# Performance work log

Hardware: AMD Instinct MI355X
Metric: run time of the kernel (lower is better)

The kernel has to match this reference:

```python
import jax, jax.numpy as jnp
import numpy as np

B = 32
N_IN = 65536
N_OUT = 65536
NNZ = 2097152  # ~32 connections per output unit


def setup_inputs() -> dict:
    key = jax.random.key(0)
    k_x, k_w, k_r, k_c = jax.random.split(key, 4)
    x = jax.random.normal(k_x, (B, N_IN), dtype=jnp.float32)
    # weight init mirrors torch: randn * (init_scale / sqrt(mean_fan_in))
    init_scale = 0.01
    fan_in_mean = float(NNZ) / float(N_OUT)
    weight = jax.random.normal(k_w, (NNZ,), dtype=jnp.float32) * (init_scale / np.sqrt(fan_in_mean))
    bias = jnp.zeros((N_OUT,), dtype=jnp.float32)
    # rows are sorted (concatenated per output j in the original __init__)
    rows = jnp.sort(jax.random.randint(k_r, (NNZ,), 0, N_OUT, dtype=jnp.int64))
    cols = jax.random.randint(k_c, (NNZ,), 0, N_IN, dtype=jnp.int64)
    return {"x": x, "weight": weight, "bias": bias, "rows": rows, "cols": cols, "N_out": N_OUT}


def reference(x, weight, bias, rows, cols, N_out):
    # gather input columns per connection, scale by per-edge weight: (B, nnz)
    weighted = x[:, cols] * weight[None, :]
    # batched scatter-add by output row: segment_sum over edges -> (N_out, B) -> (B, N_out)
    out = jax.ops.segment_sum(weighted.T, rows, num_segments=N_out,
                              indices_are_sorted=True).T
    return out + bias[None, :]
```

## Files before the change

### kernel.cpp

```cpp
#include <hip/hip_runtime.h>


typedef unsigned int u32;

static __device__ __forceinline__ u32 f2bf_bits(float f) {
  u32 b = __builtin_bit_cast(u32, f);
  return (b + 0x7fffu + ((b >> 16) & 1u)) >> 16;
}
static __device__ __forceinline__ float bf_lo(u32 u) {
  return __builtin_bit_cast(float, u << 16);
}
static __device__ __forceinline__ float bf_hi(u32 u) {
  return __builtin_bit_cast(float, u & 0xffff0000u);
}

__global__ __launch_bounds__(256) void prep_kernel(
    const float* __restrict__ x, u32* __restrict__ xTb,
    const int* __restrict__ rows, int* __restrict__ row_ptr,
    int n_in, int n_out, int nnz, int tblocks) {
  if ((int)blockIdx.x < tblocks) {
    __shared__ float t[32][65];
    int c0 = blockIdx.x * 64;
    if (c0 + 64 <= n_in) {
      const float4* x4 = (const float4*)x;
      for (int idx = threadIdx.x; idx < 32 * 16; idx += 256) {
        int b = idx >> 4, q = idx & 15;
        float4 v = x4[((size_t)b * n_in + c0) / 4 + q];
        t[b][q * 4 + 0] = v.x; t[b][q * 4 + 1] = v.y;
        t[b][q * 4 + 2] = v.z; t[b][q * 4 + 3] = v.w;
      }
    } else {
      for (int idx = threadIdx.x; idx < 32 * 64; idx += 256) {
        int b = idx >> 6, cl = idx & 63;
        int c = c0 + cl;
        t[b][cl] = (c < n_in) ? x[(size_t)b * n_in + c] : 0.f;
      }
    }
    __syncthreads();
    for (int idx = threadIdx.x; idx < 64 * 16; idx += 256) {
      int cl = idx >> 4, bp = idx & 15;
      int c = c0 + cl;
      if (c < n_in) {
        u32 v = f2bf_bits(t[2 * bp][cl]) | (f2bf_bits(t[2 * bp + 1][cl]) << 16);
        xTb[(size_t)c * 16 + bp] = v;
      }
    }
  } else {
    int j = ((int)blockIdx.x - tblocks) * 256 + threadIdx.x;
    if (j <= n_out) {
      int lo = 0, hi = nnz;
      while (lo < hi) { int m = (lo + hi) >> 1; if (rows[m] < j) lo = m + 1; else hi = m; }
      row_ptr[j] = lo;
    }
  }
}

__global__ __launch_bounds__(256) void ll_main_bf16_kernel(
    const uint4* __restrict__ xTb4,
    const float* __restrict__ wgt,
    const float4* __restrict__ bias4,
    const int* __restrict__ cols,
    const int* __restrict__ row_ptr,
    float4* __restrict__ out4, int n_out) {
  __shared__ float tile[32][65];
  int tid = threadIdx.x;
  int g = tid >> 2;
  int l = tid & 3;
  int jb = blockIdx.x * 64;
  int j = jb + g;
  float a0 = 0, a1 = 0, a2 = 0, a3 = 0, a4 = 0, a5 = 0, a6 = 0, a7 = 0;
  if (j < n_out) {
    int s = row_ptr[j], e = row_ptr[j + 1];
    int last = e - 1;
    for (int base = s; base < e; base += 8) {
      int i1 = min(base + 1, last), i2 = min(base + 2, last), i3 = min(base + 3, last);
      int i4 = min(base + 4, last), i5 = min(base + 5, last), i6 = min(base + 6, last);
      int i7 = min(base + 7, last);
      int c0 = cols[base], c1 = cols[i1], c2 = cols[i2], c3 = cols[i3];
      int c4 = cols[i4], c5 = cols[i5], c6 = cols[i6], c7 = cols[i7];
      float w0 = wgt[base];
      float w1 = (base + 1 <= last) ? wgt[i1] : 0.f;
      float w2 = (base + 2 <= last) ? wgt[i2] : 0.f;
      float w3 = (base + 3 <= last) ? wgt[i3] : 0.f;
      float w4 = (base + 4 <= last) ? wgt[i4] : 0.f;
      float w5 = (base + 5 <= last) ? wgt[i5] : 0.f;
      float w6 = (base + 6 <= last) ? wgt[i6] : 0.f;
      float w7 = (base + 7 <= last) ? wgt[i7] : 0.f;
      uint4 v0 = xTb4[(size_t)c0 * 4 + l];
      uint4 v1 = xTb4[(size_t)c1 * 4 + l];
      uint4 v2 = xTb4[(size_t)c2 * 4 + l];
      uint4 v3 = xTb4[(size_t)c3 * 4 + l];
      uint4 v4 = xTb4[(size_t)c4 * 4 + l];
      uint4 v5 = xTb4[(size_t)c5 * 4 + l];
      uint4 v6 = xTb4[(size_t)c6 * 4 + l];
      uint4 v7 = xTb4[(size_t)c7 * 4 + l];
#define EDGE(V, W) \
      a0 = fmaf(W, bf_lo(V.x), a0); a1 = fmaf(W, bf_hi(V.x), a1); \
      a2 = fmaf(W, bf_lo(V.y), a2); a3 = fmaf(W, bf_hi(V.y), a3); \
      a4 = fmaf(W, bf_lo(V.z), a4); a5 = fmaf(W, bf_hi(V.z), a5); \
      a6 = fmaf(W, bf_lo(V.w), a6); a7 = fmaf(W, bf_hi(V.w), a7);
      EDGE(v0, w0) EDGE(v1, w1) EDGE(v2, w2) EDGE(v3, w3)
      EDGE(v4, w4) EDGE(v5, w5) EDGE(v6, w6) EDGE(v7, w7)
#undef EDGE
    }
  }
  int b0 = l * 8;
  tile[b0 + 0][g] = a0; tile[b0 + 1][g] = a1; tile[b0 + 2][g] = a2; tile[b0 + 3][g] = a3;
  tile[b0 + 4][g] = a4; tile[b0 + 5][g] = a5; tile[b0 + 6][g] = a6; tile[b0 + 7][g] = a7;
  __syncthreads();
  for (int slot = tid; slot < 32 * 16; slot += 256) {
    int bb = slot >> 4, q = slot & 15;
    int jj = jb + q * 4;
    if (jj + 3 < n_out) {
      float4 bv = bias4[jj / 4];
      float4 o;
      o.x = tile[bb][q * 4 + 0] + bv.x;
      o.y = tile[bb][q * 4 + 1] + bv.y;
      o.z = tile[bb][q * 4 + 2] + bv.z;
      o.w = tile[bb][q * 4 + 3] + bv.w;
      out4[((size_t)bb * n_out + jj) / 4] = o;
    } else {
      float* out = (float*)out4;
      const float* bias = (const float*)bias4;
      for (int d = 0; d < 4; ++d)
        if (jj + d < n_out)
          out[(size_t)bb * n_out + jj + d] = tile[bb][q * 4 + d] + bias[jj + d];
    }
  }
}

__global__ __launch_bounds__(256) void transpose_x_kernel(
    const float* __restrict__ x, float* __restrict__ xT, int n_in) {
  __shared__ float t[32][65];
  int c0 = blockIdx.x * 64;
  for (int idx = threadIdx.x; idx < 32 * 64; idx += 256) {
    int b = idx >> 6, cl = idx & 63;
    int c = c0 + cl;
    t[b][cl] = (c < n_in) ? x[(size_t)b * n_in + c] : 0.0f;
  }
  __syncthreads();
  for (int idx = threadIdx.x; idx < 64 * 32; idx += 256) {
    int cl = idx >> 5, b = idx & 31;
    int c = c0 + cl;
    if (c < n_in) xT[(size_t)c * 32 + b] = t[b][cl];
  }
}

__global__ __launch_bounds__(256) void build_rowptr_bs_kernel(
    const int* __restrict__ rows, int* __restrict__ row_ptr, int nnz, int n_out) {
  int j = blockIdx.x * blockDim.x + threadIdx.x;
  if (j > n_out) return;
  int lo = 0, hi = nnz;
  while (lo < hi) { int m = (lo + hi) >> 1; if (rows[m] < j) lo = m + 1; else hi = m; }
  row_ptr[j] = lo;
}

__global__ __launch_bounds__(256) void ll_main4_kernel(
    const float4* __restrict__ xT4,
    const float* __restrict__ wgt,
    const float* __restrict__ bias,
    const int* __restrict__ cols,
    const int* __restrict__ row_ptr,
    float* __restrict__ out, int n_out) {
  __shared__ float tile[32][33];
  int tid = threadIdx.x;
  int g = tid >> 3;
  int l = tid & 7;
  int jb = blockIdx.x * 32;
  int j = jb + g;
  float ax = 0.f, ay = 0.f, az = 0.f, aw = 0.f;
  if (j < n_out) {
    int s = row_ptr[j];
    int e = row_ptr[j + 1];
    for (int base = s; base < e; base += 4) {
      int last = e - 1;
      int i1 = min(base + 1, last), i2 = min(base + 2, last), i3 = min(base + 3, last);
      int c0 = cols[base], c1 = cols[i1], c2 = cols[i2], c3 = cols[i3];
      float w0 = wgt[base];
      float w1 = (base + 1 <= last) ? wgt[i1] : 0.f;
      float w2 = (base + 2 <= last) ? wgt[i2] : 0.f;
      float w3 = (base + 3 <= last) ? wgt[i3] : 0.f;
      float4 x0 = xT4[(size_t)c0 * 8 + l];
      float4 x1 = xT4[(size_t)c1 * 8 + l];
      float4 x2 = xT4[(size_t)c2 * 8 + l];
      float4 x3 = xT4[(size_t)c3 * 8 + l];
      ax = fmaf(w0, x0.x, ax); ay = fmaf(w0, x0.y, ay);
      az = fmaf(w0, x0.z, az); aw = fmaf(w0, x0.w, aw);
      ax = fmaf(w1, x1.x, ax); ay = fmaf(w1, x1.y, ay);
      az = fmaf(w1, x1.z, az); aw = fmaf(w1, x1.w, aw);
      ax = fmaf(w2, x2.x, ax); ay = fmaf(w2, x2.y, ay);
      az = fmaf(w2, x2.z, az); aw = fmaf(w2, x2.w, aw);
      ax = fmaf(w3, x3.x, ax); ay = fmaf(w3, x3.y, ay);
      az = fmaf(w3, x3.z, az); aw = fmaf(w3, x3.w, aw);
    }
  }
  tile[l * 4 + 0][g] = ax;
  tile[l * 4 + 1][g] = ay;
  tile[l * 4 + 2][g] = az;
  tile[l * 4 + 3][g] = aw;
  __syncthreads();
  for (int idx = tid; idx < 32 * 32; idx += 256) {
    int bb = idx >> 5, jl = idx & 31;
    int jj = jb + jl;
    if (jj < n_out) out[(size_t)bb * n_out + jj] = tile[bb][jl] + bias[jj];
  }
}

__global__ __launch_bounds__(256) void ll_naive_kernel(
    const float* __restrict__ x,
    const float* __restrict__ wgt,
    const float* __restrict__ bias,
    const int* __restrict__ rows,
    const int* __restrict__ cols,
    float* __restrict__ out,
    int n_in, int n_out, int nnz, int B) {
  int idx = blockIdx.x * blockDim.x + threadIdx.x;
  if (idx >= n_out * B) return;
  int j = idx % n_out;
  int b = idx / n_out;
  int lo = 0, hi = nnz;
  while (lo < hi) { int m = (lo + hi) >> 1; if (rows[m] < j) lo = m + 1; else hi = m; }
  int s = lo;
  hi = nnz;
  while (lo < hi) { int m = (lo + hi) >> 1; if (rows[m] <= j) lo = m + 1; else hi = m; }
  int e = lo;
  float acc = 0.0f;
  for (int t = s; t < e; ++t)
    acc = fmaf(wgt[t], x[(size_t)b * n_in + cols[t]], acc);
  out[(size_t)b * n_out + j] = acc + bias[j];
}

extern "C" void kernel_launch(void* const* d_in, const int* in_sizes, int n_in_arrays,
                              void* d_out, int out_size, void* d_ws, size_t ws_size,
                              hipStream_t stream) {
  const float* x    = (const float*)d_in[0];
  const float* wgt  = (const float*)d_in[1];
  const float* bias = (const float*)d_in[2];
  const int*   rows = (const int*)d_in[3];
  const int*   cols = (const int*)d_in[4];
  float* out = (float*)d_out;

  const int nnz   = in_sizes[1];
  const int n_out = in_sizes[2];
  const int B     = out_size / n_out;
  const int n_in  = in_sizes[0] / B;

  const size_t xTb_bytes = (size_t)n_in * 32 * 2;
  const size_t xT_bytes  = (size_t)n_in * 32 * sizeof(float);
  const size_t rp_bytes  = (size_t)(n_out + 1) * sizeof(int);

  if (B == 32 && ws_size >= xTb_bytes + rp_bytes) {
    u32* xTb = (u32*)d_ws;
    int* row_ptr = (int*)((char*)d_ws + xTb_bytes);
    int tblocks = (n_in + 63) / 64;
    int rblocks = (n_out + 1 + 255) / 256;
    prep_kernel<<<tblocks + rblocks, 256, 0, stream>>>(
        x, xTb, rows, row_ptr, n_in, n_out, nnz, tblocks);
    ll_main_bf16_kernel<<<(n_out + 63) / 64, 256, 0, stream>>>(
        (const uint4*)xTb, wgt, (const float4*)bias, cols, row_ptr,
        (float4*)out, n_out);
  } else if (B == 32 && ws_size >= xT_bytes + rp_bytes) {
    float* xT = (float*)d_ws;
    int* row_ptr = (int*)((char*)d_ws + xT_bytes);
    transpose_x_kernel<<<(n_in + 63) / 64, 256, 0, stream>>>(x, xT, n_in);
    build_rowptr_bs_kernel<<<(n_out + 256) / 256, 256, 0, stream>>>(rows, row_ptr, nnz, n_out);
    ll_main4_kernel<<<(n_out + 31) / 32, 256, 0, stream>>>(
        (const float4*)xT, wgt, bias, cols, row_ptr, out, n_out);
  } else {
    int total = n_out * B;
    ll_naive_kernel<<<(total + 255) / 256, 256, 0, stream>>>(
        x, wgt, bias, rows, cols, out, n_in, n_out, nnz, B);
  }
}
```

Measured before the change: 43.99 us.

## Split edge loop across two wave halves, shuffle-broadcast indices, edge-parallel rowptr build

The row_ptr construction changes from a binary search per output to an edge-parallel pass in which each edge writes the boundaries between its row and the previous row. The main kernel moves to 512 threads. Two half-blocks each process alternating groups of 4 edges, and their partial sums are combined through shared memory. Each lane now loads one col and one weight and broadcasts them with shuffles, which replaces the 8 redundant loads per lane. This raises memory-level parallelism and cuts redundant index traffic, at the cost of an extra shared-memory reduction and barrier, plus more prep blocks.

```diff
diff --git a/kernel.cpp b/kernel.cpp
--- a/kernel.cpp
+++ b/kernel.cpp
@@ -46,16 +46,18 @@
       }
     }
   } else {
-    int j = ((int)blockIdx.x - tblocks) * 256 + threadIdx.x;
-    if (j <= n_out) {
-      int lo = 0, hi = nnz;
-      while (lo < hi) { int m = (lo + hi) >> 1; if (rows[m] < j) lo = m + 1; else hi = m; }
-      row_ptr[j] = lo;
-    }
-  }
-}
-
-__global__ __launch_bounds__(256) void ll_main_bf16_kernel(
+    int e = ((int)blockIdx.x - tblocks) * 256 + threadIdx.x;
+    if (e < nnz) {
+      int r = rows[e];
+      int rp = (e == 0) ? -1 : rows[e - 1];
+      for (int j = rp + 1; j <= r; ++j) row_ptr[j] = e;
+      if (e == nnz - 1)
+        for (int j = r + 1; j <= n_out; ++j) row_ptr[j] = nnz;
+    }
+  }
+}
+
+__global__ __launch_bounds__(512, 8) void ll_main_bf16_kernel(
     const uint4* __restrict__ xTb4,
     const float* __restrict__ wgt,
     const float4* __restrict__ bias4,
@@ -64,52 +66,48 @@
     float4* __restrict__ out4, int n_out) {
   __shared__ float tile[32][65];
   int tid = threadIdx.x;
-  int g = tid >> 2;
-  int l = tid & 3;
+  int lane = tid & 63;
+  int l = lane & 3;
+  int gw = lane >> 2;
+  int wv = tid >> 6;
+  int half = wv >> 2;
+  int g = (wv & 3) * 16 + gw;
+  int gb = lane & 60;
   int jb = blockIdx.x * 64;
   int j = jb + g;
   float a0 = 0, a1 = 0, a2 = 0, a3 = 0, a4 = 0, a5 = 0, a6 = 0, a7 = 0;
   if (j < n_out) {
     int s = row_ptr[j], e = row_ptr[j + 1];
     int last = e - 1;
-    for (int base = s; base < e; base += 8) {
-      int i1 = min(base + 1, last), i2 = min(base + 2, last), i3 = min(base + 3, last);
-      int i4 = min(base + 4, last), i5 = min(base + 5, last), i6 = min(base + 6, last);
-      int i7 = min(base + 7, last);
-      int c0 = cols[base], c1 = cols[i1], c2 = cols[i2], c3 = cols[i3];
-      int c4 = cols[i4], c5 = cols[i5], c6 = cols[i6], c7 = cols[i7];
-      float w0 = wgt[base];
-      float w1 = (base + 1 <= last) ? wgt[i1] : 0.f;
-      float w2 = (base + 2 <= last) ? wgt[i2] : 0.f;
-      float w3 = (base + 3 <= last) ? wgt[i3] : 0.f;
-      float w4 = (base + 4 <= last) ? wgt[i4] : 0.f;
-      float w5 = (base + 5 <= last) ? wgt[i5] : 0.f;
-      float w6 = (base + 6 <= last) ? wgt[i6] : 0.f;
-      float w7 = (base + 7 <= last) ? wgt[i7] : 0.f;
-      uint4 v0 = xTb4[(size_t)c0 * 4 + l];
-      uint4 v1 = xTb4[(size_t)c1 * 4 + l];
-      uint4 v2 = xTb4[(size_t)c2 * 4 + l];
-      uint4 v3 = xTb4[(size_t)c3 * 4 + l];
-      uint4 v4 = xTb4[(size_t)c4 * 4 + l];
-      uint4 v5 = xTb4[(size_t)c5 * 4 + l];
-      uint4 v6 = xTb4[(size_t)c6 * 4 + l];
-      uint4 v7 = xTb4[(size_t)c7 * 4 + l];
-#define EDGE(V, W) \
-      a0 = fmaf(W, bf_lo(V.x), a0); a1 = fmaf(W, bf_hi(V.x), a1); \
-      a2 = fmaf(W, bf_lo(V.y), a2); a3 = fmaf(W, bf_hi(V.y), a3); \
-      a4 = fmaf(W, bf_lo(V.z), a4); a5 = fmaf(W, bf_hi(V.z), a5); \
-      a6 = fmaf(W, bf_lo(V.w), a6); a7 = fmaf(W, bf_hi(V.w), a7);
-      EDGE(v0, w0) EDGE(v1, w1) EDGE(v2, w2) EDGE(v3, w3)
-      EDGE(v4, w4) EDGE(v5, w5) EDGE(v6, w6) EDGE(v7, w7)
-#undef EDGE
+    for (int base = s + half * 4; base < e; base += 8) {
+      int il = min(base + l, last);
+      int cl_ = cols[il];
+      float wl_ = (base + l <= last) ? wgt[il] : 0.f;
+#define EDGE_K(K) { \
+      int   ck = __shfl(cl_, gb | K); \
+      float wk = __shfl(wl_, gb | K); \
+      uint4 v  = xTb4[(size_t)ck * 4 + l]; \
+      a0 = fmaf(wk, bf_lo(v.x), a0); a1 = fmaf(wk, bf_hi(v.x), a1); \
+      a2 = fmaf(wk, bf_lo(v.y), a2); a3 = fmaf(wk, bf_hi(v.y), a3); \
+      a4 = fmaf(wk, bf_lo(v.z), a4); a5 = fmaf(wk, bf_hi(v.z), a5); \
+      a6 = fmaf(wk, bf_lo(v.w), a6); a7 = fmaf(wk, bf_hi(v.w), a7); }
+      EDGE_K(0) EDGE_K(1) EDGE_K(2) EDGE_K(3)
+#undef EDGE_K
     }
   }
   int b0 = l * 8;
-  tile[b0 + 0][g] = a0; tile[b0 + 1][g] = a1; tile[b0 + 2][g] = a2; tile[b0 + 3][g] = a3;
-  tile[b0 + 4][g] = a4; tile[b0 + 5][g] = a5; tile[b0 + 6][g] = a6; tile[b0 + 7][g] = a7;
-  __syncthreads();
-  for (int slot = tid; slot < 32 * 16; slot += 256) {
-    int bb = slot >> 4, q = slot & 15;
+  if (half == 0) {
+    tile[b0 + 0][g] = a0; tile[b0 + 1][g] = a1; tile[b0 + 2][g] = a2; tile[b0 + 3][g] = a3;
+    tile[b0 + 4][g] = a4; tile[b0 + 5][g] = a5; tile[b0 + 6][g] = a6; tile[b0 + 7][g] = a7;
+  }
+  __syncthreads();
+  if (half == 1) {
+    tile[b0 + 0][g] += a0; tile[b0 + 1][g] += a1; tile[b0 + 2][g] += a2; tile[b0 + 3][g] += a3;
+    tile[b0 + 4][g] += a4; tile[b0 + 5][g] += a5; tile[b0 + 6][g] += a6; tile[b0 + 7][g] += a7;
+  }
+  __syncthreads();
+  {
+    int bb = tid >> 4, q = tid & 15;
     int jj = jb + q * 4;
     if (jj + 3 < n_out) {
       float4 bv = bias4[jj / 4];
@@ -253,10 +251,10 @@
     u32* xTb = (u32*)d_ws;
     int* row_ptr = (int*)((char*)d_ws + xTb_bytes);
     int tblocks = (n_in + 63) / 64;
-    int rblocks = (n_out + 1 + 255) / 256;
-    prep_kernel<<<tblocks + rblocks, 256, 0, stream>>>(
+    int eblocks = (nnz + 255) / 256;
+    prep_kernel<<<tblocks + eblocks, 256, 0, stream>>>(
         x, xTb, rows, row_ptr, n_in, n_out, nnz, tblocks);
-    ll_main_bf16_kernel<<<(n_out + 63) / 64, 256, 0, stream>>>(
+    ll_main_bf16_kernel<<<(n_out + 63) / 64, 512, 0, stream>>>(
         (const uint4*)xTb, wgt, (const float4*)bias, cols, row_ptr,
         (float4*)out, n_out);
   } else if (B == 32 && ws_size >= xT_bytes + rp_bytes) {
```

Measured after the change: 37.84 us, median of 2. 1.16x faster.
